# Kernel optimization log

Measured on AMD Instinct MI355X. Metric: run time of the kernel, lower is better.

Reference implementation:

```python
import jax, jax.numpy as jnp
import numpy as np

N_NODES = 100000
N_EDGES = 3200000
IN_C = 128
OUT_C = 40
NEG_SLOPE = 0.2


def _p(key, shape, scale=0.1):
    return jax.random.normal(key, shape, dtype=jnp.float32) * scale


def setup_inputs() -> dict:
    key = jax.random.key(0)
    ks = jax.random.split(key, 16)
    x = jax.random.normal(ks[0], (N_NODES, IN_C), dtype=jnp.float32)
    edge_index = jax.random.randint(ks[1], (2, N_EDGES), 0, N_NODES, dtype=jnp.int32)
    # layer 1: in=128 -> heads=4, out=4 (concat -> 16)
    W1 = _p(ks[2], (IN_C, 4 * 4))
    a_src1 = _p(ks[3], (4, 4))
    a_dst1 = _p(ks[4], (4, 4))
    b1 = jnp.zeros((16,), jnp.float32)
    # layer 2: 16 -> heads=8, out=8 (concat -> 64)
    W2 = _p(ks[5], (16, 8 * 8))
    a_src2 = _p(ks[6], (8, 8))
    a_dst2 = _p(ks[7], (8, 8))
    b2 = jnp.zeros((64,), jnp.float32)
    # layer 3: 64 -> heads=1, out=OUT_C, concat=False
    W3 = _p(ks[8], (64, OUT_C))
    a_src3 = _p(ks[9], (1, OUT_C))
    a_dst3 = _p(ks[10], (1, OUT_C))
    b3 = jnp.zeros((OUT_C,), jnp.float32)
    return {"x": x, "edge_index": edge_index,
            "W1": W1, "a_src1": a_src1, "a_dst1": a_dst1, "b1": b1,
            "W2": W2, "a_src2": a_src2, "a_dst2": a_dst2, "b2": b2,
            "W3": W3, "a_src3": a_src3, "a_dst3": a_dst3, "b3": b3}


def gat_conv(x, src, dst, W, a_src, a_dst, b, heads, out_c, concat):
    # x: [N, F_in]; src/dst: [E] (self loops already included)
    N = x.shape[0]
    h = (x @ W).reshape(N, heads, out_c)                 # [N, H, C]
    e_src = jnp.sum(h * a_src, axis=-1)                  # [N, H]
    e_dst = jnp.sum(h * a_dst, axis=-1)                  # [N, H]
    e = jax.nn.leaky_relu(e_src[src] + e_dst[dst], NEG_SLOPE)  # [E, H]
    # segment softmax over edges grouped by destination node
    m = jax.ops.segment_max(e, dst, num_segments=N)      # [N, H]
    ex = jnp.exp(e - m[dst])
    s = jax.ops.segment_sum(ex, dst, num_segments=N)
    alpha = ex / (s[dst] + 1e-16)                        # [E, H]
    out = jax.ops.segment_sum(h[src] * alpha[:, :, None], dst, num_segments=N)  # [N, H, C]
    out = out.reshape(N, heads * out_c) if concat else out.mean(axis=1)
    return out + b


def reference(x, edge_index, W1, a_src1, a_dst1, b1, W2, a_src2, a_dst2, b2, W3, a_src3, a_dst3, b3):
    N = x.shape[0]
    loops = jnp.arange(N, dtype=edge_index.dtype)
    src = jnp.concatenate([edge_index[0], loops])
    dst = jnp.concatenate([edge_index[1], loops])
    h = jax.nn.elu(gat_conv(x, src, dst, W1, a_src1, a_dst1, b1, 4, 4, True))
    h = jax.nn.elu(gat_conv(h, src, dst, W2, a_src2, a_dst2, b2, 8, 8, True))
    out = gat_conv(h, src, dst, W3, a_src3, a_dst3, b3, 1, OUT_C, False)
    return out
```

## Files before the change

### kernel.cpp

```cpp
#include <hip/hip_runtime.h>

#define NN 100000
#define NE 3200000
#define ET (NE + NN)
#define NEG_SLOPE 0.2f
#define BSH 7
#define WIN (1 << BSH)
#define NBUC ((NN + WIN - 1) >> BSH)
#define NBLK 1024
#define EPB ((ET + NBLK - 1) / NBLK)

__device__ __forceinline__ float lrelu(float v) { return v > 0.f ? v : NEG_SLOPE * v; }

__device__ __forceinline__ unsigned short f2bf(float x) {
    unsigned u = __float_as_uint(x);
    return (unsigned short)((u + 0x7fffu + ((u >> 16) & 1u)) >> 16);
}
__device__ __forceinline__ float bflo(unsigned u) { return __uint_as_float(u << 16); }
__device__ __forceinline__ float bfhi(unsigned u) { return __uint_as_float(u & 0xffff0000u); }


__global__ __launch_bounds__(256) void cnt_kernel(const int* __restrict__ dst,
                                                  int* __restrict__ cnt) {
    __shared__ int h[NBUC];
    for (int i = threadIdx.x; i < NBUC; i += 256) h[i] = 0;
    __syncthreads();
    int lo = blockIdx.x * EPB;
    int hi = lo + EPB; if (hi > ET) hi = ET;
    for (int k = lo + threadIdx.x; k < hi; k += 256) {
        int d = (k < NE) ? dst[k] : k - NE;
        atomicAdd(&h[d >> BSH], 1);
    }
    __syncthreads();
    for (int i = threadIdx.x; i < NBUC; i += 256)
        cnt[i * NBLK + blockIdx.x] = h[i];
}

__global__ __launch_bounds__(256) void rowsum_kernel(const int* __restrict__ cnt,
                                                     int* __restrict__ tot) {
    int wave = threadIdx.x >> 6, lane = threadIdx.x & 63;
    int b = blockIdx.x * 4 + wave;
    if (b >= NBUC) return;
    int s = 0;
#pragma unroll
    for (int j = 0; j < NBLK / 256; ++j) {
        int4 v = ((const int4*)(cnt + b * NBLK))[lane + 64 * j];
        s += v.x + v.y + v.z + v.w;
    }
#pragma unroll
    for (int off = 32; off; off >>= 1) s += __shfl_xor(s, off);
    if (lane == 0) tot[b] = s;
}

__global__ __launch_bounds__(1024) void scan_kernel(const int* __restrict__ tot,
                                                    int* __restrict__ bstart) {
    __shared__ int t[1024];
    int b = threadIdx.x;
    int s = (b < NBUC) ? tot[b] : 0;
    t[b] = s;
    __syncthreads();
    for (int off = 1; off < 1024; off <<= 1) {
        int v = (b >= off) ? t[b - off] : 0;
        __syncthreads();
        t[b] += v;
        __syncthreads();
    }
    if (b < NBUC) bstart[b] = t[b] - s;
    if (b == 0) bstart[NBUC] = ET;
}

__global__ __launch_bounds__(256) void base_kernel(int* __restrict__ cnt,
                                                   const int* __restrict__ bstart) {
    int wave = threadIdx.x >> 6, lane = threadIdx.x & 63;
    int b = blockIdx.x * 4 + wave;
    if (b >= NBUC) return;
    int run = bstart[b];
    for (int c0 = 0; c0 < NBLK; c0 += 64) {
        int v = cnt[b * NBLK + c0 + lane];
        int x = v;
#pragma unroll
        for (int off = 1; off < 64; off <<= 1) {
            int y = __shfl_up(x, off);
            if (lane >= off) x += y;
        }
        cnt[b * NBLK + c0 + lane] = run + x - v;
        run += __shfl(x, 63);
    }
}

__global__ __launch_bounds__(256) void scatter_kernel(const int* __restrict__ src,
                                                      const int* __restrict__ dst,
                                                      const int* __restrict__ base,
                                                      unsigned* __restrict__ tmpp) {
    __shared__ int loff[NBUC];
    for (int i = threadIdx.x; i < NBUC; i += 256) loff[i] = base[i * NBLK + blockIdx.x];
    __syncthreads();
    int lo = blockIdx.x * EPB;
    int hi = lo + EPB; if (hi > ET) hi = ET;
    for (int k = lo + threadIdx.x; k < hi; k += 256) {
        int s, d;
        if (k < NE) { s = src[k]; d = dst[k]; }
        else { s = d = k - NE; }
        int p = atomicAdd(&loff[d >> BSH], 1);
        tmpp[p] = (unsigned)s | ((unsigned)(d & (WIN - 1)) << 17);
    }
}

__global__ __launch_bounds__(256) void sort_kernel(const int* __restrict__ bstart,
                                                   const unsigned* __restrict__ tmpp,
                                                   int* __restrict__ rowptr,
                                                   int* __restrict__ ssrc) {
    __shared__ int hist[WIN];
    __shared__ int scan[WIN];
    __shared__ int cur[WIN];
    int buc = blockIdx.x;
    int nlo = buc << BSH;
    int nwin = NN - nlo; if (nwin > WIN) nwin = WIN;
    int lo = bstart[buc], hi = bstart[buc + 1];
    int tid = threadIdx.x;
    if (tid < WIN) hist[tid] = 0;
    __syncthreads();
    for (int k = lo + tid; k < hi; k += 256)
        atomicAdd(&hist[tmpp[k] >> 17], 1);
    __syncthreads();
    if (tid < WIN) scan[tid] = hist[tid];
    __syncthreads();
    for (int off = 1; off < WIN; off <<= 1) {
        int v = (tid >= off && tid < WIN) ? scan[tid - off] : 0;
        __syncthreads();
        if (tid < WIN) scan[tid] += v;
        __syncthreads();
    }
    if (tid < WIN) {
        int ex = scan[tid] - hist[tid];
        cur[tid] = ex;
        if (tid < nwin) rowptr[nlo + tid] = lo + ex;
    }
    if (buc == 0 && tid == 0) rowptr[NN] = ET;
    __syncthreads();
    for (int k = lo + tid; k < hi; k += 256) {
        unsigned e = tmpp[k];
        int p = atomicAdd(&cur[e >> 17], 1);
        ssrc[lo + p] = (int)(e & 0x1FFFFu);
    }
}


template <int FIN, int FOUT, int C>
__global__ __launch_bounds__(256) void gemm_attn_kernel(
    const float* __restrict__ x, const float* __restrict__ W,
    const float* __restrict__ a_src, const float* __restrict__ a_dst,
    unsigned short* __restrict__ h, float* __restrict__ esrc,
    float* __restrict__ edst, int N) {
    constexpr int HH = FOUT / C;
    constexpr int F4 = FOUT / 4;
    constexpr int TPH = C / 4;
    __shared__ __align__(16) float Ws[FIN * FOUT];
    for (int i = threadIdx.x; i < FIN * FOUT; i += blockDim.x) Ws[i] = W[i];
    __syncthreads();
    int idx = blockIdx.x * blockDim.x + threadIdx.x;
    if (idx >= N * F4) return;
    int n = idx / F4, f4 = idx - n * F4;
    int fb = 4 * f4;
    const float4* xr = (const float4*)(x + (long)n * FIN);
    float a0 = 0.f, a1 = 0.f, a2 = 0.f, a3 = 0.f;
#pragma unroll
    for (int k4 = 0; k4 < FIN / 4; ++k4) {
        float4 xv = xr[k4];
        const float* wr = &Ws[(4 * k4) * FOUT + fb];
        float4 w0 = *(const float4*)(wr);
        float4 w1 = *(const float4*)(wr + FOUT);
        float4 w2 = *(const float4*)(wr + 2 * FOUT);
        float4 w3 = *(const float4*)(wr + 3 * FOUT);
        a0 = fmaf(xv.x, w0.x, a0); a1 = fmaf(xv.x, w0.y, a1);
        a2 = fmaf(xv.x, w0.z, a2); a3 = fmaf(xv.x, w0.w, a3);
        a0 = fmaf(xv.y, w1.x, a0); a1 = fmaf(xv.y, w1.y, a1);
        a2 = fmaf(xv.y, w1.z, a2); a3 = fmaf(xv.y, w1.w, a3);
        a0 = fmaf(xv.z, w2.x, a0); a1 = fmaf(xv.z, w2.y, a1);
        a2 = fmaf(xv.z, w2.z, a2); a3 = fmaf(xv.z, w2.w, a3);
        a0 = fmaf(xv.w, w3.x, a0); a1 = fmaf(xv.w, w3.y, a1);
        a2 = fmaf(xv.w, w3.z, a2); a3 = fmaf(xv.w, w3.w, a3);
    }
    unsigned short b0 = f2bf(a0), b1 = f2bf(a1), b2 = f2bf(a2), b3 = f2bf(a3);
    *(ushort4*)(h + (long)n * FOUT + fb) = make_ushort4(b0, b1, b2, b3);
    float q0 = bflo((unsigned)b0), q1 = bflo((unsigned)b1);
    float q2 = bflo((unsigned)b2), q3 = bflo((unsigned)b3);
    float vs = q0 * a_src[fb] + q1 * a_src[fb + 1] + q2 * a_src[fb + 2] + q3 * a_src[fb + 3];
    float vd = q0 * a_dst[fb] + q1 * a_dst[fb + 1] + q2 * a_dst[fb + 2] + q3 * a_dst[fb + 3];
#pragma unroll
    for (int o = 1; o < TPH; o <<= 1) {
        vs += __shfl_xor(vs, o);
        vd += __shfl_xor(vd, o);
    }
    if ((f4 % TPH) == 0) {
        int hh = f4 / TPH;
        esrc[n * HH + hh] = vs;
        edst[n * HH + hh] = vd;
    }
}

template <int FIN, int FOUT, int SO>
__global__ __launch_bounds__(256) void gemm_kernel(const float* __restrict__ x,
                                                   const float* __restrict__ W,
                                                   unsigned short* __restrict__ h, int N) {
    constexpr int F4 = FOUT / 4;
    __shared__ __align__(16) float Ws[FIN * FOUT];
    for (int i = threadIdx.x; i < FIN * FOUT; i += blockDim.x) Ws[i] = W[i];
    __syncthreads();
    int idx = blockIdx.x * blockDim.x + threadIdx.x;
    if (idx >= N * F4) return;
    int n = idx / F4, f4 = idx - n * F4;
    int fb = 4 * f4;
    const float4* xr = (const float4*)(x + (long)n * FIN);
    float a0 = 0.f, a1 = 0.f, a2 = 0.f, a3 = 0.f;
#pragma unroll
    for (int k4 = 0; k4 < FIN / 4; ++k4) {
        float4 xv = xr[k4];
        const float* wr = &Ws[(4 * k4) * FOUT + fb];
        float4 w0 = *(const float4*)(wr);
        float4 w1 = *(const float4*)(wr + FOUT);
        float4 w2 = *(const float4*)(wr + 2 * FOUT);
        float4 w3 = *(const float4*)(wr + 3 * FOUT);
        a0 = fmaf(xv.x, w0.x, a0); a1 = fmaf(xv.x, w0.y, a1);
        a2 = fmaf(xv.x, w0.z, a2); a3 = fmaf(xv.x, w0.w, a3);
        a0 = fmaf(xv.y, w1.x, a0); a1 = fmaf(xv.y, w1.y, a1);
        a2 = fmaf(xv.y, w1.z, a2); a3 = fmaf(xv.y, w1.w, a3);
        a0 = fmaf(xv.z, w2.x, a0); a1 = fmaf(xv.z, w2.y, a1);
        a2 = fmaf(xv.z, w2.z, a2); a3 = fmaf(xv.z, w2.w, a3);
        a0 = fmaf(xv.w, w3.x, a0); a1 = fmaf(xv.w, w3.y, a1);
        a2 = fmaf(xv.w, w3.z, a2); a3 = fmaf(xv.w, w3.w, a3);
    }
    *(ushort4*)(h + (long)n * SO + fb) = make_ushort4(f2bf(a0), f2bf(a1), f2bf(a2), f2bf(a3));
}

template <int C, int SO>
__global__ void attn_kernel(const unsigned short* __restrict__ h,
                            const float* __restrict__ a_src,
                            const float* __restrict__ a_dst, float* __restrict__ esrc,
                            float* __restrict__ edst, int N) {
    int idx = blockIdx.x * blockDim.x + threadIdx.x;
    if (idx >= N) return;
    const uint4* hp = (const uint4*)(h + (long)idx * SO);
    float s = 0.f, d = 0.f;
#pragma unroll
    for (int c8 = 0; c8 < C / 8; ++c8) {
        uint4 v = hp[c8];
        int c = 8 * c8;
        s += bflo(v.x) * a_src[c] + bfhi(v.x) * a_src[c + 1];
        d += bflo(v.x) * a_dst[c] + bfhi(v.x) * a_dst[c + 1];
        s += bflo(v.y) * a_src[c + 2] + bfhi(v.y) * a_src[c + 3];
        d += bflo(v.y) * a_dst[c + 2] + bfhi(v.y) * a_dst[c + 3];
        s += bflo(v.z) * a_src[c + 4] + bfhi(v.z) * a_src[c + 5];
        d += bflo(v.z) * a_dst[c + 4] + bfhi(v.z) * a_dst[c + 5];
        s += bflo(v.w) * a_src[c + 6] + bfhi(v.w) * a_src[c + 7];
        d += bflo(v.w) * a_dst[c + 6] + bfhi(v.w) * a_dst[c + 7];
    }
    esrc[idx] = s;
    edst[idx] = d;
}

template <int H, int C, int L, int G, int NPW, int FPL, int RSL, int U, bool ELU>
__global__ __launch_bounds__(256) void agg_kernel(
    const int* __restrict__ rowptr, const int* __restrict__ ssrc,
    const float* __restrict__ esrc, const float* __restrict__ edst,
    const unsigned short* __restrict__ hbuf, const float* __restrict__ b,
    float* __restrict__ out, int N) {
    constexpr int F = H * C;
    constexpr int AQ = (F + FPL - 1) / FPL;
    constexpr int S = L * G;
    static_assert(S * NPW == 64, "wave layout");
    static_assert(AQ <= L, "lanes cover features");
    int lane = threadIdx.x & 63;
    int wave = threadIdx.x >> 6;
    int sub = lane / S;
    int ls = lane - sub * S;
    int g = ls / L, q = ls - g * L;
    int n = (blockIdx.x * 4 + wave) * NPW + sub;
    if (n >= N) return;
    const bool act = (q < AQ);
    int h = act ? (FPL * q) / C : 0;
    int qa = act ? q : 0;
    float edn = edst[n * H + h];
    int beg = rowptr[n], end = rowptr[n + 1];
    int kend = end - 1;
    float sum = 0.f;
    float acc[FPL];
#pragma unroll
    for (int i = 0; i < FPL; ++i) acc[i] = 0.f;

    int k = beg + g;
    int ss[U];
#pragma unroll
    for (int u = 0; u < U; ++u) {
        int kk = k + u * G;
        ss[u] = ssrc[kk < kend ? kk : kend];
    }
    while (k < end) {
        uint4 hv4[U];
        uint2 hv2[U];
        float es[U];
#pragma unroll
        for (int u = 0; u < U; ++u) {
            if constexpr (FPL == 8) hv4[u] = ((const uint4*)hbuf)[ss[u] * RSL + qa];
            else hv2[u] = ((const uint2*)hbuf)[ss[u] * RSL + qa];
            es[u] = esrc[ss[u] * H + h];
        }
        int kn = k + U * G;
        int sn[U];
#pragma unroll
        for (int u = 0; u < U; ++u) {
            int kk = kn + u * G;
            sn[u] = ssrc[kk < kend ? kk : kend];
        }
        __builtin_amdgcn_sched_barrier(0);
#pragma unroll
        for (int u = 0; u < U; ++u) {
            float ex = (act && (k + u * G < end)) ? __expf(lrelu(es[u] + edn)) : 0.f;
            if constexpr (FPL == 8) {
                uint4 v = hv4[u];
                acc[0] = fmaf(ex, bflo(v.x), acc[0]); acc[1] = fmaf(ex, bfhi(v.x), acc[1]);
                acc[2] = fmaf(ex, bflo(v.y), acc[2]); acc[3] = fmaf(ex, bfhi(v.y), acc[3]);
                acc[4] = fmaf(ex, bflo(v.z), acc[4]); acc[5] = fmaf(ex, bfhi(v.z), acc[5]);
                acc[6] = fmaf(ex, bflo(v.w), acc[6]); acc[7] = fmaf(ex, bfhi(v.w), acc[7]);
            } else {
                uint2 v = hv2[u];
                acc[0] = fmaf(ex, bflo(v.x), acc[0]); acc[1] = fmaf(ex, bfhi(v.x), acc[1]);
                acc[2] = fmaf(ex, bflo(v.y), acc[2]); acc[3] = fmaf(ex, bfhi(v.y), acc[3]);
            }
            sum += ex;
        }
#pragma unroll
        for (int u = 0; u < U; ++u) ss[u] = sn[u];
        k = kn;
    }
#pragma unroll
    for (int step = L; step < S; step <<= 1) {
        sum += __shfl_xor(sum, step);
#pragma unroll
        for (int i = 0; i < FPL; ++i) acc[i] += __shfl_xor(acc[i], step);
    }
    if (g == 0 && act) {
        float inv = 1.f / (sum + 1e-16f);
        float v[FPL];
#pragma unroll
        for (int i = 0; i < FPL; ++i) {
            v[i] = acc[i] * inv + b[FPL * q + i];
            if (ELU) v[i] = v[i] > 0.f ? v[i] : __expf(v[i]) - 1.f;
        }
        float* op = out + n * F + FPL * q;
#pragma unroll
        for (int i = 0; i < FPL; i += 4)
            *(float4*)(op + i) = make_float4(v[i], v[i + 1], v[i + 2], v[i + 3]);
    }
}

static inline int cdiv(long a, int b) { return (int)((a + b - 1) / b); }

extern "C" void kernel_launch(void* const* d_in, const int* in_sizes, int n_in,
                              void* d_out, int out_size, void* d_ws, size_t ws_size,
                              hipStream_t stream) {
    const float* x1 = (const float*)d_in[0];
    const int* ei = (const int*)d_in[1];
    const int* src = ei;
    const int* dst = ei + NE;
    const float* W1 = (const float*)d_in[2];
    const float* as1 = (const float*)d_in[3];
    const float* ad1 = (const float*)d_in[4];
    const float* b1 = (const float*)d_in[5];
    const float* W2 = (const float*)d_in[6];
    const float* as2 = (const float*)d_in[7];
    const float* ad2 = (const float*)d_in[8];
    const float* b2 = (const float*)d_in[9];
    const float* W3 = (const float*)d_in[10];
    const float* as3 = (const float*)d_in[11];
    const float* ad3 = (const float*)d_in[12];
    const float* b3 = (const float*)d_in[13];
    float* out = (float*)d_out;

    char* wsb = (char*)d_ws;
    unsigned short* hbuf = (unsigned short*)wsb;  wsb += (long)NN * 64 * 2;
    float* x2 = (float*)wsb;         wsb += (long)NN * 16 * 4;
    float* x3 = (float*)wsb;         wsb += (long)NN * 64 * 4;
    float* esrc = (float*)wsb;       wsb += (long)NN * 8 * 4;
    float* edst = (float*)wsb;       wsb += (long)NN * 8 * 4;
    unsigned* tmpp = (unsigned*)wsb; wsb += (long)ET * 4;
    int* ssrc = (int*)wsb;           wsb += (long)ET * 4;
    int* rowptr = (int*)wsb;         wsb += (long)(NN + 1) * 4;
    int* cnt = (int*)wsb;            wsb += (long)NBUC * NBLK * 4;
    int* bstart = (int*)wsb;         wsb += (long)(NBUC + 1) * 4;
    int* tot = (int*)wsb;            wsb += (long)NBUC * 4;

    const int B = 256;

    cnt_kernel<<<NBLK, B, 0, stream>>>(dst, cnt);
    rowsum_kernel<<<cdiv(NBUC, 4), B, 0, stream>>>(cnt, tot);
    scan_kernel<<<1, 1024, 0, stream>>>(tot, bstart);
    base_kernel<<<cdiv(NBUC, 4), B, 0, stream>>>(cnt, bstart);
    scatter_kernel<<<NBLK, B, 0, stream>>>(src, dst, cnt, tmpp);
    sort_kernel<<<NBUC, B, 0, stream>>>(bstart, tmpp, rowptr, ssrc);

    gemm_attn_kernel<128, 16, 4><<<cdiv((long)NN * 4, B), B, 0, stream>>>(
        x1, W1, as1, ad1, hbuf, esrc, edst, NN);
    agg_kernel<4, 4, 4, 8, 2, 4, 4, 5, true><<<cdiv(NN, 8), B, 0, stream>>>(
        rowptr, ssrc, esrc, edst, hbuf, b1, x2, NN);

    gemm_attn_kernel<16, 64, 8><<<cdiv((long)NN * 16, B), B, 0, stream>>>(
        x2, W2, as2, ad2, hbuf, esrc, edst, NN);
    agg_kernel<8, 8, 8, 8, 1, 8, 8, 5, true><<<cdiv(NN, 4), B, 0, stream>>>(
        rowptr, ssrc, esrc, edst, hbuf, b2, x3, NN);

    gemm_kernel<64, 40, 40><<<cdiv((long)NN * 10, B), B, 0, stream>>>(x3, W3, hbuf, NN);
    attn_kernel<40, 40><<<cdiv(NN, B), B, 0, stream>>>(hbuf, as3, ad3, esrc, edst, NN);
    agg_kernel<1, 40, 8, 8, 1, 8, 5, 5, false><<<cdiv(NN, 4), B, 0, stream>>>(
        rowptr, ssrc, esrc, edst, hbuf, b3, out, NN);
}
```

Baseline: 450.1 us.

## Split layer-2 aggregation into four head-group passes for cache locality

```diff
diff --git a/kernel.cpp b/kernel.cpp
--- a/kernel.cpp
+++ b/kernel.cpp
@@ -259,15 +259,17 @@
     edst[idx] = d;
 }
 
-template <int H, int C, int L, int G, int NPW, int FPL, int RSL, int U, bool ELU>
+template <int HT, int HOFF, int H, int C, int L, int G, int NPW, int FPL, int RSL, int U, bool ELU>
 __global__ __launch_bounds__(256) void agg_kernel(
     const int* __restrict__ rowptr, const int* __restrict__ ssrc,
     const float* __restrict__ esrc, const float* __restrict__ edst,
     const unsigned short* __restrict__ hbuf, const float* __restrict__ b,
     float* __restrict__ out, int N) {
     constexpr int F = H * C;
-    constexpr int AQ = (F + FPL - 1) / FPL;
+    constexpr int FT = HT * C;
+    constexpr int AQ = F / FPL;
     constexpr int S = L * G;
+    constexpr int QOFF = (HOFF * C) / FPL;
     static_assert(S * NPW == 64, "wave layout");
     static_assert(AQ <= L, "lanes cover features");
     int lane = threadIdx.x & 63;
@@ -278,9 +280,9 @@
     int n = (blockIdx.x * 4 + wave) * NPW + sub;
     if (n >= N) return;
     const bool act = (q < AQ);
-    int h = act ? (FPL * q) / C : 0;
+    int h = HOFF + (act ? (FPL * q) / C : 0);
     int qa = act ? q : 0;
-    float edn = edst[n * H + h];
+    float edn = edst[n * HT + h];
     int beg = rowptr[n], end = rowptr[n + 1];
     int kend = end - 1;
     float sum = 0.f;
@@ -301,9 +303,9 @@
         float es[U];
 #pragma unroll
         for (int u = 0; u < U; ++u) {
-            if constexpr (FPL == 8) hv4[u] = ((const uint4*)hbuf)[ss[u] * RSL + qa];
-            else hv2[u] = ((const uint2*)hbuf)[ss[u] * RSL + qa];
-            es[u] = esrc[ss[u] * H + h];
+            if constexpr (FPL == 8) hv4[u] = ((const uint4*)hbuf)[ss[u] * RSL + QOFF + qa];
+            else hv2[u] = ((const uint2*)hbuf)[ss[u] * RSL + QOFF + qa];
+            es[u] = esrc[ss[u] * HT + h];
         }
         int kn = k + U * G;
         int sn[U];
@@ -344,10 +346,10 @@
         float v[FPL];
 #pragma unroll
         for (int i = 0; i < FPL; ++i) {
-            v[i] = acc[i] * inv + b[FPL * q + i];
+            v[i] = acc[i] * inv + b[HOFF * C + FPL * q + i];
             if (ELU) v[i] = v[i] > 0.f ? v[i] : __expf(v[i]) - 1.f;
         }
-        float* op = out + n * F + FPL * q;
+        float* op = out + (long)n * FT + HOFF * C + FPL * q;
 #pragma unroll
         for (int i = 0; i < FPL; i += 4)
             *(float4*)(op + i) = make_float4(v[i], v[i + 1], v[i + 2], v[i + 3]);
@@ -401,16 +403,22 @@
 
     gemm_attn_kernel<128, 16, 4><<<cdiv((long)NN * 4, B), B, 0, stream>>>(
         x1, W1, as1, ad1, hbuf, esrc, edst, NN);
-    agg_kernel<4, 4, 4, 8, 2, 4, 4, 5, true><<<cdiv(NN, 8), B, 0, stream>>>(
+    agg_kernel<4, 0, 4, 4, 4, 8, 2, 4, 4, 5, true><<<cdiv(NN, 8), B, 0, stream>>>(
         rowptr, ssrc, esrc, edst, hbuf, b1, x2, NN);
 
     gemm_attn_kernel<16, 64, 8><<<cdiv((long)NN * 16, B), B, 0, stream>>>(
         x2, W2, as2, ad2, hbuf, esrc, edst, NN);
-    agg_kernel<8, 8, 8, 8, 1, 8, 8, 5, true><<<cdiv(NN, 4), B, 0, stream>>>(
+    agg_kernel<8, 0, 2, 8, 2, 8, 4, 8, 8, 5, true><<<cdiv(NN, 16), B, 0, stream>>>(
+        rowptr, ssrc, esrc, edst, hbuf, b2, x3, NN);
+    agg_kernel<8, 2, 2, 8, 2, 8, 4, 8, 8, 5, true><<<cdiv(NN, 16), B, 0, stream>>>(
+        rowptr, ssrc, esrc, edst, hbuf, b2, x3, NN);
+    agg_kernel<8, 4, 2, 8, 2, 8, 4, 8, 8, 5, true><<<cdiv(NN, 16), B, 0, stream>>>(
+        rowptr, ssrc, esrc, edst, hbuf, b2, x3, NN);
+    agg_kernel<8, 6, 2, 8, 2, 8, 4, 8, 8, 5, true><<<cdiv(NN, 16), B, 0, stream>>>(
         rowptr, ssrc, esrc, edst, hbuf, b2, x3, NN);
 
     gemm_kernel<64, 40, 40><<<cdiv((long)NN * 10, B), B, 0, stream>>>(x3, W3, hbuf, NN);
     attn_kernel<40, 40><<<cdiv(NN, B), B, 0, stream>>>(hbuf, as3, ad3, esrc, edst, NN);
-    agg_kernel<1, 40, 8, 8, 1, 8, 5, 5, false><<<cdiv(NN, 4), B, 0, stream>>>(
+    agg_kernel<1, 0, 1, 40, 8, 8, 1, 8, 5, 5, false><<<cdiv(NN, 4), B, 0, stream>>>(
         rowptr, ssrc, esrc, edst, hbuf, b3, out, NN);
 }
```

After: 682.3 us. 1.52x slower.

## Split layer-2/3 feature buffers into column slices and aggregate per slice

Applied to the files above, without the earlier changes.

```diff
diff --git a/kernel.cpp b/kernel.cpp
--- a/kernel.cpp
+++ b/kernel.cpp
@@ -146,7 +146,7 @@
 }
 
 
-template <int FIN, int FOUT, int C>
+template <int FIN, int FOUT, int C, int SLICEF>
 __global__ __launch_bounds__(256) void gemm_attn_kernel(
     const float* __restrict__ x, const float* __restrict__ W,
     const float* __restrict__ a_src, const float* __restrict__ a_dst,
@@ -182,7 +182,12 @@
         a2 = fmaf(xv.w, w3.z, a2); a3 = fmaf(xv.w, w3.w, a3);
     }
     unsigned short b0 = f2bf(a0), b1 = f2bf(a1), b2 = f2bf(a2), b3 = f2bf(a3);
-    *(ushort4*)(h + (long)n * FOUT + fb) = make_ushort4(b0, b1, b2, b3);
+    long hoff;
+    if constexpr (SLICEF > 0)
+        hoff = (long)(fb / SLICEF) * ((long)N * SLICEF) + (long)n * SLICEF + (fb % SLICEF);
+    else
+        hoff = (long)n * FOUT + fb;
+    *(ushort4*)(h + hoff) = make_ushort4(b0, b1, b2, b3);
     float q0 = bflo((unsigned)b0), q1 = bflo((unsigned)b1);
     float q2 = bflo((unsigned)b2), q3 = bflo((unsigned)b3);
     float vs = q0 * a_src[fb] + q1 * a_src[fb + 1] + q2 * a_src[fb + 2] + q3 * a_src[fb + 3];
@@ -199,7 +204,7 @@
     }
 }
 
-template <int FIN, int FOUT, int SO>
+template <int FIN, int FOUT, int SLICEF>
 __global__ __launch_bounds__(256) void gemm_kernel(const float* __restrict__ x,
                                                    const float* __restrict__ W,
                                                    unsigned short* __restrict__ h, int N) {
@@ -230,43 +235,46 @@
         a0 = fmaf(xv.w, w3.x, a0); a1 = fmaf(xv.w, w3.y, a1);
         a2 = fmaf(xv.w, w3.z, a2); a3 = fmaf(xv.w, w3.w, a3);
     }
-    *(ushort4*)(h + (long)n * SO + fb) = make_ushort4(f2bf(a0), f2bf(a1), f2bf(a2), f2bf(a3));
-}
-
-template <int C, int SO>
-__global__ void attn_kernel(const unsigned short* __restrict__ h,
-                            const float* __restrict__ a_src,
-                            const float* __restrict__ a_dst, float* __restrict__ esrc,
-                            float* __restrict__ edst, int N) {
+    long hoff;
+    if constexpr (SLICEF > 0)
+        hoff = (long)(fb / SLICEF) * ((long)N * SLICEF) + (long)n * SLICEF + (fb % SLICEF);
+    else
+        hoff = (long)n * FOUT + fb;
+    *(ushort4*)(h + hoff) = make_ushort4(f2bf(a0), f2bf(a1), f2bf(a2), f2bf(a3));
+}
+
+__global__ void attn3_kernel(const unsigned short* __restrict__ h,
+                             const float* __restrict__ a_src,
+                             const float* __restrict__ a_dst, float* __restrict__ esrc,
+                             float* __restrict__ edst, int N) {
     int idx = blockIdx.x * blockDim.x + threadIdx.x;
     if (idx >= N) return;
-    const uint4* hp = (const uint4*)(h + (long)idx * SO);
     float s = 0.f, d = 0.f;
 #pragma unroll
-    for (int c8 = 0; c8 < C / 8; ++c8) {
-        uint4 v = hp[c8];
-        int c = 8 * c8;
-        s += bflo(v.x) * a_src[c] + bfhi(v.x) * a_src[c + 1];
-        d += bflo(v.x) * a_dst[c] + bfhi(v.x) * a_dst[c + 1];
-        s += bflo(v.y) * a_src[c + 2] + bfhi(v.y) * a_src[c + 3];
-        d += bflo(v.y) * a_dst[c + 2] + bfhi(v.y) * a_dst[c + 3];
-        s += bflo(v.z) * a_src[c + 4] + bfhi(v.z) * a_src[c + 5];
-        d += bflo(v.z) * a_dst[c + 4] + bfhi(v.z) * a_dst[c + 5];
-        s += bflo(v.w) * a_src[c + 6] + bfhi(v.w) * a_src[c + 7];
-        d += bflo(v.w) * a_dst[c + 6] + bfhi(v.w) * a_dst[c + 7];
+    for (int sl = 0; sl < 2; ++sl) {
+        const uint2* hp = (const uint2*)(h + (long)sl * N * 20 + (long)idx * 20);
+#pragma unroll
+        for (int j = 0; j < 5; ++j) {
+            uint2 v = hp[j];
+            int c = sl * 20 + 4 * j;
+            s += bflo(v.x) * a_src[c] + bfhi(v.x) * a_src[c + 1];
+            d += bflo(v.x) * a_dst[c] + bfhi(v.x) * a_dst[c + 1];
+            s += bflo(v.y) * a_src[c + 2] + bfhi(v.y) * a_src[c + 3];
+            d += bflo(v.y) * a_dst[c + 2] + bfhi(v.y) * a_dst[c + 3];
+        }
     }
     esrc[idx] = s;
     edst[idx] = d;
 }
 
-template <int H, int C, int L, int G, int NPW, int FPL, int RSL, int U, bool ELU>
+template <int FT, int FOFF, int F, int C, int L, int G, int NPW, int FPL, int RSL, int U, bool ELU>
 __global__ __launch_bounds__(256) void agg_kernel(
     const int* __restrict__ rowptr, const int* __restrict__ ssrc,
     const float* __restrict__ esrc, const float* __restrict__ edst,
     const unsigned short* __restrict__ hbuf, const float* __restrict__ b,
     float* __restrict__ out, int N) {
-    constexpr int F = H * C;
-    constexpr int AQ = (F + FPL - 1) / FPL;
+    constexpr int HT = FT / C;
+    constexpr int AQ = F / FPL;
     constexpr int S = L * G;
     static_assert(S * NPW == 64, "wave layout");
     static_assert(AQ <= L, "lanes cover features");
@@ -278,9 +286,9 @@
     int n = (blockIdx.x * 4 + wave) * NPW + sub;
     if (n >= N) return;
     const bool act = (q < AQ);
-    int h = act ? (FPL * q) / C : 0;
+    int h = (FOFF + (act ? FPL * q : 0)) / C;
     int qa = act ? q : 0;
-    float edn = edst[n * H + h];
+    float edn = edst[n * HT + h];
     int beg = rowptr[n], end = rowptr[n + 1];
     int kend = end - 1;
     float sum = 0.f;
@@ -303,7 +311,7 @@
         for (int u = 0; u < U; ++u) {
             if constexpr (FPL == 8) hv4[u] = ((const uint4*)hbuf)[ss[u] * RSL + qa];
             else hv2[u] = ((const uint2*)hbuf)[ss[u] * RSL + qa];
-            es[u] = esrc[ss[u] * H + h];
+            es[u] = esrc[ss[u] * HT + h];
         }
         int kn = k + U * G;
         int sn[U];
@@ -344,10 +352,10 @@
         float v[FPL];
 #pragma unroll
         for (int i = 0; i < FPL; ++i) {
-            v[i] = acc[i] * inv + b[FPL * q + i];
+            v[i] = acc[i] * inv + b[FOFF + FPL * q + i];
             if (ELU) v[i] = v[i] > 0.f ? v[i] : __expf(v[i]) - 1.f;
         }
-        float* op = out + n * F + FPL * q;
+        float* op = out + (long)n * FT + FOFF + FPL * q;
 #pragma unroll
         for (int i = 0; i < FPL; i += 4)
             *(float4*)(op + i) = make_float4(v[i], v[i + 1], v[i + 2], v[i + 3]);
@@ -399,18 +407,26 @@
     scatter_kernel<<<NBLK, B, 0, stream>>>(src, dst, cnt, tmpp);
     sort_kernel<<<NBUC, B, 0, stream>>>(bstart, tmpp, rowptr, ssrc);
 
-    gemm_attn_kernel<128, 16, 4><<<cdiv((long)NN * 4, B), B, 0, stream>>>(
+    gemm_attn_kernel<128, 16, 4, 0><<<cdiv((long)NN * 4, B), B, 0, stream>>>(
         x1, W1, as1, ad1, hbuf, esrc, edst, NN);
-    agg_kernel<4, 4, 4, 8, 2, 4, 4, 5, true><<<cdiv(NN, 8), B, 0, stream>>>(
+    agg_kernel<16, 0, 16, 4, 4, 8, 2, 4, 4, 5, true><<<cdiv(NN, 8), B, 0, stream>>>(
         rowptr, ssrc, esrc, edst, hbuf, b1, x2, NN);
 
-    gemm_attn_kernel<16, 64, 8><<<cdiv((long)NN * 16, B), B, 0, stream>>>(
+    gemm_attn_kernel<16, 64, 8, 16><<<cdiv((long)NN * 16, B), B, 0, stream>>>(
         x2, W2, as2, ad2, hbuf, esrc, edst, NN);
-    agg_kernel<8, 8, 8, 8, 1, 8, 8, 5, true><<<cdiv(NN, 4), B, 0, stream>>>(
-        rowptr, ssrc, esrc, edst, hbuf, b2, x3, NN);
-
-    gemm_kernel<64, 40, 40><<<cdiv((long)NN * 10, B), B, 0, stream>>>(x3, W3, hbuf, NN);
-    attn_kernel<40, 40><<<cdiv(NN, B), B, 0, stream>>>(hbuf, as3, ad3, esrc, edst, NN);
-    agg_kernel<1, 40, 8, 8, 1, 8, 5, 5, false><<<cdiv(NN, 4), B, 0, stream>>>(
-        rowptr, ssrc, esrc, edst, hbuf, b3, out, NN);
-}
+    agg_kernel<64, 0, 16, 8, 2, 8, 4, 8, 2, 5, true><<<cdiv(NN, 16), B, 0, stream>>>(
+        rowptr, ssrc, esrc, edst, hbuf + 0L * NN * 16, b2, x3, NN);
+    agg_kernel<64, 16, 16, 8, 2, 8, 4, 8, 2, 5, true><<<cdiv(NN, 16), B, 0, stream>>>(
+        rowptr, ssrc, esrc, edst, hbuf + 1L * NN * 16, b2, x3, NN);
+    agg_kernel<64, 32, 16, 8, 2, 8, 4, 8, 2, 5, true><<<cdiv(NN, 16), B, 0, stream>>>(
+        rowptr, ssrc, esrc, edst, hbuf + 2L * NN * 16, b2, x3, NN);
+    agg_kernel<64, 48, 16, 8, 2, 8, 4, 8, 2, 5, true><<<cdiv(NN, 16), B, 0, stream>>>(
+        rowptr, ssrc, esrc, edst, hbuf + 3L * NN * 16, b2, x3, NN);
+
+    gemm_kernel<64, 40, 20><<<cdiv((long)NN * 10, B), B, 0, stream>>>(x3, W3, hbuf, NN);
+    attn3_kernel<<<cdiv(NN, B), B, 0, stream>>>(hbuf, as3, ad3, esrc, edst, NN);
+    agg_kernel<40, 0, 20, 40, 8, 8, 1, 4, 5, 5, false><<<cdiv(NN, 4), B, 0, stream>>>(
+        rowptr, ssrc, esrc, edst, hbuf + 0L * NN * 20, b3, out, NN);
+    agg_kernel<40, 20, 20, 40, 8, 8, 1, 4, 5, 5, false><<<cdiv(NN, 4), B, 0, stream>>>(
+        rowptr, ssrc, esrc, edst, hbuf + 1L * NN * 20, b3, out, NN);
+}
```

After: 621.6 us. +38.1%, slower.

## Build CSR via global per-node atomic histogram instead of two-level bucket sort

Applied to the files above, without the earlier changes.

```diff
diff --git a/kernel.cpp b/kernel.cpp
--- a/kernel.cpp
+++ b/kernel.cpp
@@ -4,11 +4,6 @@
 #define NE 3200000
 #define ET (NE + NN)
 #define NEG_SLOPE 0.2f
-#define BSH 7
-#define WIN (1 << BSH)
-#define NBUC ((NN + WIN - 1) >> BSH)
-#define NBLK 1024
-#define EPB ((ET + NBLK - 1) / NBLK)
 
 __device__ __forceinline__ float lrelu(float v) { return v > 0.f ? v : NEG_SLOPE * v; }
 
@@ -20,128 +15,74 @@
 __device__ __forceinline__ float bfhi(unsigned u) { return __uint_as_float(u & 0xffff0000u); }
 
 
-__global__ __launch_bounds__(256) void cnt_kernel(const int* __restrict__ dst,
-                                                  int* __restrict__ cnt) {
-    __shared__ int h[NBUC];
-    for (int i = threadIdx.x; i < NBUC; i += 256) h[i] = 0;
-    __syncthreads();
-    int lo = blockIdx.x * EPB;
-    int hi = lo + EPB; if (hi > ET) hi = ET;
-    for (int k = lo + threadIdx.x; k < hi; k += 256) {
-        int d = (k < NE) ? dst[k] : k - NE;
-        atomicAdd(&h[d >> BSH], 1);
-    }
-    __syncthreads();
-    for (int i = threadIdx.x; i < NBUC; i += 256)
-        cnt[i * NBLK + blockIdx.x] = h[i];
-}
-
-__global__ __launch_bounds__(256) void rowsum_kernel(const int* __restrict__ cnt,
+__global__ __launch_bounds__(256) void initdeg_kernel(int* __restrict__ deg) {
+    int n = blockIdx.x * 256 + threadIdx.x;
+    if (n < NN) deg[n] = 1;
+}
+
+__global__ __launch_bounds__(256) void deg_kernel(const int* __restrict__ dst,
+                                                  int* __restrict__ deg) {
+    int stride = gridDim.x * 256;
+    for (int k = blockIdx.x * 256 + threadIdx.x; k < NE; k += stride)
+        atomicAdd(&deg[dst[k]], 1);
+}
+
+__global__ __launch_bounds__(1024) void scan1_kernel(const int* __restrict__ deg,
+                                                     int* __restrict__ rowptr,
                                                      int* __restrict__ tot) {
-    int wave = threadIdx.x >> 6, lane = threadIdx.x & 63;
-    int b = blockIdx.x * 4 + wave;
-    if (b >= NBUC) return;
-    int s = 0;
-#pragma unroll
-    for (int j = 0; j < NBLK / 256; ++j) {
-        int4 v = ((const int4*)(cnt + b * NBLK))[lane + 64 * j];
-        s += v.x + v.y + v.z + v.w;
-    }
-#pragma unroll
-    for (int off = 32; off; off >>= 1) s += __shfl_xor(s, off);
-    if (lane == 0) tot[b] = s;
-}
-
-__global__ __launch_bounds__(1024) void scan_kernel(const int* __restrict__ tot,
-                                                    int* __restrict__ bstart) {
     __shared__ int t[1024];
-    int b = threadIdx.x;
-    int s = (b < NBUC) ? tot[b] : 0;
-    t[b] = s;
+    int n = blockIdx.x * 1024 + threadIdx.x;
+    int s = (n < NN) ? deg[n] : 0;
+    t[threadIdx.x] = s;
     __syncthreads();
     for (int off = 1; off < 1024; off <<= 1) {
-        int v = (b >= off) ? t[b - off] : 0;
+        int v = (threadIdx.x >= off) ? t[threadIdx.x - off] : 0;
         __syncthreads();
-        t[b] += v;
+        t[threadIdx.x] += v;
         __syncthreads();
     }
-    if (b < NBUC) bstart[b] = t[b] - s;
-    if (b == 0) bstart[NBUC] = ET;
-}
-
-__global__ __launch_bounds__(256) void base_kernel(int* __restrict__ cnt,
-                                                   const int* __restrict__ bstart) {
-    int wave = threadIdx.x >> 6, lane = threadIdx.x & 63;
-    int b = blockIdx.x * 4 + wave;
-    if (b >= NBUC) return;
-    int run = bstart[b];
-    for (int c0 = 0; c0 < NBLK; c0 += 64) {
-        int v = cnt[b * NBLK + c0 + lane];
-        int x = v;
-#pragma unroll
-        for (int off = 1; off < 64; off <<= 1) {
-            int y = __shfl_up(x, off);
-            if (lane >= off) x += y;
-        }
-        cnt[b * NBLK + c0 + lane] = run + x - v;
-        run += __shfl(x, 63);
-    }
-}
-
-__global__ __launch_bounds__(256) void scatter_kernel(const int* __restrict__ src,
-                                                      const int* __restrict__ dst,
-                                                      const int* __restrict__ base,
-                                                      unsigned* __restrict__ tmpp) {
-    __shared__ int loff[NBUC];
-    for (int i = threadIdx.x; i < NBUC; i += 256) loff[i] = base[i * NBLK + blockIdx.x];
+    if (n <= NN && n < (blockIdx.x + 1) * 1024)
+        if (n < NN) rowptr[n] = t[threadIdx.x] - s;
+    if (threadIdx.x == 1023) tot[blockIdx.x] = t[1023];
+}
+
+__global__ __launch_bounds__(128) void scan2_kernel(int* __restrict__ tot, int nb) {
+    __shared__ int t[128];
+    int i = threadIdx.x;
+    int s = (i < nb) ? tot[i] : 0;
+    t[i] = s;
     __syncthreads();
-    int lo = blockIdx.x * EPB;
-    int hi = lo + EPB; if (hi > ET) hi = ET;
-    for (int k = lo + threadIdx.x; k < hi; k += 256) {
-        int s, d;
-        if (k < NE) { s = src[k]; d = dst[k]; }
-        else { s = d = k - NE; }
-        int p = atomicAdd(&loff[d >> BSH], 1);
-        tmpp[p] = (unsigned)s | ((unsigned)(d & (WIN - 1)) << 17);
-    }
-}
-
-__global__ __launch_bounds__(256) void sort_kernel(const int* __restrict__ bstart,
-                                                   const unsigned* __restrict__ tmpp,
-                                                   int* __restrict__ rowptr,
+    for (int off = 1; off < 128; off <<= 1) {
+        int v = (i >= off) ? t[i - off] : 0;
+        __syncthreads();
+        t[i] += v;
+        __syncthreads();
+    }
+    if (i < nb) tot[i] = t[i] - s;
+}
+
+__global__ __launch_bounds__(1024) void scan3_kernel(int* __restrict__ rowptr,
+                                                     const int* __restrict__ tot,
+                                                     int* __restrict__ cur,
+                                                     int* __restrict__ ssrc) {
+    int n = blockIdx.x * 1024 + threadIdx.x;
+    if (n >= NN) return;
+    int r = rowptr[n] + tot[blockIdx.x];
+    rowptr[n] = r;
+    ssrc[r] = n;
+    cur[n] = r + 1;
+    if (n == 0) rowptr[NN] = ET;
+}
+
+__global__ __launch_bounds__(256) void fill_kernel(const int* __restrict__ src,
+                                                   const int* __restrict__ dst,
+                                                   int* __restrict__ cur,
                                                    int* __restrict__ ssrc) {
-    __shared__ int hist[WIN];
-    __shared__ int scan[WIN];
-    __shared__ int cur[WIN];
-    int buc = blockIdx.x;
-    int nlo = buc << BSH;
-    int nwin = NN - nlo; if (nwin > WIN) nwin = WIN;
-    int lo = bstart[buc], hi = bstart[buc + 1];
-    int tid = threadIdx.x;
-    if (tid < WIN) hist[tid] = 0;
-    __syncthreads();
-    for (int k = lo + tid; k < hi; k += 256)
-        atomicAdd(&hist[tmpp[k] >> 17], 1);
-    __syncthreads();
-    if (tid < WIN) scan[tid] = hist[tid];
-    __syncthreads();
-    for (int off = 1; off < WIN; off <<= 1) {
-        int v = (tid >= off && tid < WIN) ? scan[tid - off] : 0;
-        __syncthreads();
-        if (tid < WIN) scan[tid] += v;
-        __syncthreads();
-    }
-    if (tid < WIN) {
-        int ex = scan[tid] - hist[tid];
-        cur[tid] = ex;
-        if (tid < nwin) rowptr[nlo + tid] = lo + ex;
-    }
-    if (buc == 0 && tid == 0) rowptr[NN] = ET;
-    __syncthreads();
-    for (int k = lo + tid; k < hi; k += 256) {
-        unsigned e = tmpp[k];
-        int p = atomicAdd(&cur[e >> 17], 1);
-        ssrc[lo + p] = (int)(e & 0x1FFFFu);
+    int stride = gridDim.x * 256;
+    for (int k = blockIdx.x * 256 + threadIdx.x; k < NE; k += stride) {
+        int s = src[k], d = dst[k];
+        int p = atomicAdd(&cur[d], 1);
+        ssrc[p] = s;
     }
 }
 
@@ -383,21 +324,21 @@
     float* x3 = (float*)wsb;         wsb += (long)NN * 64 * 4;
     float* esrc = (float*)wsb;       wsb += (long)NN * 8 * 4;
     float* edst = (float*)wsb;       wsb += (long)NN * 8 * 4;
-    unsigned* tmpp = (unsigned*)wsb; wsb += (long)ET * 4;
     int* ssrc = (int*)wsb;           wsb += (long)ET * 4;
     int* rowptr = (int*)wsb;         wsb += (long)(NN + 1) * 4;
-    int* cnt = (int*)wsb;            wsb += (long)NBUC * NBLK * 4;
-    int* bstart = (int*)wsb;         wsb += (long)(NBUC + 1) * 4;
-    int* tot = (int*)wsb;            wsb += (long)NBUC * 4;
+    int* deg = (int*)wsb;            wsb += (long)NN * 4;
+    int* cur = (int*)wsb;            wsb += (long)NN * 4;
+    int* tot = (int*)wsb;            wsb += (long)128 * 4;
 
     const int B = 256;
-
-    cnt_kernel<<<NBLK, B, 0, stream>>>(dst, cnt);
-    rowsum_kernel<<<cdiv(NBUC, 4), B, 0, stream>>>(cnt, tot);
-    scan_kernel<<<1, 1024, 0, stream>>>(tot, bstart);
-    base_kernel<<<cdiv(NBUC, 4), B, 0, stream>>>(cnt, bstart);
-    scatter_kernel<<<NBLK, B, 0, stream>>>(src, dst, cnt, tmpp);
-    sort_kernel<<<NBUC, B, 0, stream>>>(bstart, tmpp, rowptr, ssrc);
+    const int NSB = cdiv(NN, 1024);
+
+    initdeg_kernel<<<cdiv(NN, B), B, 0, stream>>>(deg);
+    deg_kernel<<<2048, B, 0, stream>>>(dst, deg);
+    scan1_kernel<<<NSB, 1024, 0, stream>>>(deg, rowptr, tot);
+    scan2_kernel<<<1, 128, 0, stream>>>(tot, NSB);
+    scan3_kernel<<<NSB, 1024, 0, stream>>>(rowptr, tot, cur, ssrc);
+    fill_kernel<<<2048, B, 0, stream>>>(src, dst, cur, ssrc);
 
     gemm_attn_kernel<128, 16, 4><<<cdiv((long)NN * 4, B), B, 0, stream>>>(
         x1, W1, as1, ad1, hbuf, esrc, edst, NN);
```

Result: slower. 779.3 us (+73.1%).
